# Optimization experiments

Measured on AMD Instinct MI355X. Metric: run time of the kernel, lower is better.

Reference implementation:

```python
import jax, jax.numpy as jnp
import numpy as np

E = 8      # number of experts (sublayers)
N = 8192   # tokens / batch rows
D = 1024   # sublayer input size (max_sublayer_input_size)
H = 2048   # sublayer output size
O = 1024   # output_encoding_size


def setup_inputs() -> dict:
    key = jax.random.key(0)
    k0, k1, k2, k3 = jax.random.split(key, 4)
    x_feat = jax.random.normal(k0, (N, D), dtype=jnp.float32)
    expert_idx = jax.random.randint(k1, (N,), 0, E)  # exclusive (top-1) routing
    # Stacked expert params: sublayers = Linear(D,H), encoders = Linear(H,O)
    W1 = jax.random.normal(k2, (E, D, H), dtype=jnp.float32) * (1.0 / np.sqrt(D))
    b1 = jnp.zeros((E, H), dtype=jnp.float32)
    W2 = jax.random.normal(k3, (E, H, O), dtype=jnp.float32) * (1.0 / np.sqrt(H))
    b2 = jnp.zeros((E, O), dtype=jnp.float32)
    return {"x_feat": x_feat, "W1": W1, "b1": b1, "W2": W2, "b2": b2,
            "expert_idx": expert_idx}


def reference(x_feat, W1, b1, W2, b2, expert_idx):
    # one-hot sublayer_mask (last E columns of the original x)
    onehot = jax.nn.one_hot(expert_idx, E, dtype=x_feat.dtype)  # [N, E]
    # Exclusive dispatch: each token goes through exactly one expert.
    # Structural loop over the fixed E experts; combine via the one-hot mask
    # (equivalent to the original gather -> sublayer -> encoder -> scatter).
    enc = jnp.zeros((x_feat.shape[0], O), dtype=x_feat.dtype)
    for i in range(E):
        h = x_feat @ W1[i] + b1[i]          # [N, H] sublayer
        y = h @ W2[i] + b2[i]               # [N, O] encoder
        enc = enc + onehot[:, i:i + 1] * y  # keep only rows routed to expert i
    # output = [encoded (O cols) | sublayer_mask (E cols)]
    return jnp.concatenate([enc, onehot], axis=1)
```

## Files before the change

### kernel.cpp

```cpp
#include <hip/hip_runtime.h>

#define NTOK 8192
#define DDIM 1024
#define HDIM 2048
#define ODIM 1024
#define NEXP 8
#define OUTW (ODIM + NEXP)
#define MT_MAX 64

typedef __bf16 bf16_t;
typedef bf16_t bf16x8 __attribute__((ext_vector_type(8)));
typedef bf16_t bf16x4 __attribute__((ext_vector_type(4)));
typedef float f32x4 __attribute__((ext_vector_type(4)));

__device__ __forceinline__ void gld_lds16(bf16_t* lds, const bf16_t* g) {
  __builtin_amdgcn_global_load_lds(
      (__attribute__((address_space(1))) void*)g,
      (__attribute__((address_space(3))) void*)lds, 16, 0, 0);
}

__global__ void route_kernel(const int* __restrict__ idx, float* __restrict__ out,
                             int* __restrict__ rank, int* cnt) {
  __shared__ int lcnt[NEXP];
  __shared__ int lbase[NEXP];
  int t = threadIdx.x;
  if (t < NEXP) lcnt[t] = 0;
  __syncthreads();
  int n = blockIdx.x * 256 + t;
  int e = idx[n];
  int lr = atomicAdd(&lcnt[e], 1);
  __syncthreads();
  if (t < NEXP) lbase[t] = atomicAdd(&cnt[t], lcnt[t]);
  __syncthreads();
  rank[n] = lbase[e] + lr;
  float* o = out + (size_t)n * OUTW + ODIM;
#pragma unroll
  for (int j = 0; j < NEXP; j++) o[j] = (j == e) ? 1.0f : 0.0f;
}

__device__ __forceinline__ void prefix_of(const int* cnt, int e, int& base, int& count) {
  base = 0; count = 0;
#pragma unroll
  for (int j = 0; j < NEXP; j++) {
    int c = cnt[j];
    if (j < e) base += c;
    if (j == e) count = c;
  }
}

__global__ void gather_kernel(const float* __restrict__ x, const int* __restrict__ idx,
                              const int* __restrict__ rank, const int* __restrict__ cnt,
                              bf16_t* __restrict__ xg, int* __restrict__ tok_of_pos) {
  int n = blockIdx.x;
  int e = idx[n];
  int base, count;
  prefix_of(cnt, e, base, count);
  int pos = base + rank[n];
  if (threadIdx.x == 0) tok_of_pos[pos] = n;
  float4 v = ((const float4*)(x + (size_t)n * DDIM))[threadIdx.x];
  bf16x4 o;
  o[0] = (bf16_t)v.x; o[1] = (bf16_t)v.y; o[2] = (bf16_t)v.z; o[3] = (bf16_t)v.w;
  *(bf16x4*)(xg + (size_t)pos * DDIM + threadIdx.x * 4) = o;
}

__global__ __launch_bounds__(256) void wtrans2_kernel(
    const float* __restrict__ s1, bf16_t* __restrict__ d1,
    const float* __restrict__ s2, bf16_t* __restrict__ d2) {
  __shared__ float t[128][65];
  int b = blockIdx.x;
  const float* src; bf16_t* dst; int R, C, bx, by, e;
  if (b < 2048) {
    src = s1; dst = d1; R = DDIM; C = HDIM;
    bx = b & 31; by = (b >> 5) & 7; e = b >> 8;
  } else {
    int b2 = b - 2048;
    src = s2; dst = d2; R = HDIM; C = ODIM;
    bx = b2 & 15; by = (b2 >> 4) & 15; e = b2 >> 8;
  }
  int c0 = bx * 64, r0g = by * 128;
  int tid = threadIdx.x;
  const float* s = src + (size_t)e * R * C;
#pragma unroll
  for (int p = 0; p < 8; p++) {
    int r = (tid >> 4) + p * 16;
    int c4 = (tid & 15) * 4;
    float4 v = *(const float4*)&s[(size_t)(r0g + r) * C + c0 + c4];
    t[r][c4 + 0] = v.x;
    t[r][c4 + 1] = v.y;
    t[r][c4 + 2] = v.z;
    t[r][c4 + 3] = v.w;
  }
  __syncthreads();
  bf16_t* d = dst + (size_t)e * R * C;
  int w = tid >> 6, l = tid & 63;
#pragma unroll
  for (int itc = 0; itc < 2; itc++) {
#pragma unroll
    for (int it2 = 0; it2 < 2; it2++) {
      int c = (l >> 3) + 8 * w + 32 * itc;
      int r0 = (l & 7) * 8 + 64 * it2;
      bf16x8 o;
#pragma unroll
      for (int j = 0; j < 8; j++) o[j] = (bf16_t)t[r0 + j][c];
      *(bf16x8*)&d[(size_t)(c0 + c) * R + r0g + r0] = o;
    }
  }
}

template <int KDIM, int NCOLS, int MTG, bool TO_BF16>
__global__ __launch_bounds__(256) void gemm_kernel(
    const bf16_t* __restrict__ A, const bf16_t* __restrict__ Bt,
    const float* __restrict__ bias,
    const int* __restrict__ cnt,
    const int* __restrict__ tok_of_pos,
    bf16_t* __restrict__ outb, float* __restrict__ outf) {
  constexpr int NT = NCOLS / 128;
  const int b = blockIdx.x;
  const int e = b & 7;
  int t = b >> 3;
  const int mtl = t % MTG;
  t /= MTG;
  const int nt = t % NT;
  const int g = t / NT;
  const int mt = g * MTG + mtl;

  int base, count;
  prefix_of(cnt, e, base, count);
  if (mt * 128 >= count) return;

  __shared__ bf16_t lA[128 * 32];
  __shared__ bf16_t lB[128 * 32];

  const int tid = threadIdx.x;
  const int lane = tid & 63;
  const int wave = tid >> 6;
  const int mrow = lane & 15;
  const int q = lane >> 4;
  const int wm = (wave & 1) * 64;
  const int wn = (wave >> 1) * 64;

  const bf16_t* pA[2];
  const bf16_t* pB[2];
#pragma unroll
  for (int s = 0; s < 2; s++) {
    int lrow = wave * 32 + s * 16 + (lane >> 2);
    int kq = (lane & 3) ^ (lrow & 3);
    int gr = base + mt * 128 + lrow;
    if (gr > NTOK - 1) gr = NTOK - 1;
    pA[s] = A + (size_t)gr * KDIM + kq * 8;
    int nrow = nt * 128 + lrow;
    pB[s] = Bt + ((size_t)e * NCOLS + nrow) * KDIM + kq * 8;
  }

  f32x4 acc[4][4] = {};
  const bf16_t* la0 = &lA[(wm + mrow) * 32 + ((q ^ (mrow & 3)) * 8)];
  const bf16_t* lb0 = &lB[(wn + mrow) * 32 + ((q ^ (mrow & 3)) * 8)];

  for (int kk = 0; kk < KDIM; kk += 32) {
#pragma unroll
    for (int s = 0; s < 2; s++) {
      gld_lds16(&lA[(wave * 2 + s) * 512], pA[s] + kk);
      gld_lds16(&lB[(wave * 2 + s) * 512], pB[s] + kk);
    }
    __syncthreads();
    bf16x8 af[4], bfr[4];
#pragma unroll
    for (int i = 0; i < 4; i++) {
      af[i]  = *(const bf16x8*)(la0 + i * 16 * 32);
      bfr[i] = *(const bf16x8*)(lb0 + i * 16 * 32);
    }
#pragma unroll
    for (int i = 0; i < 4; i++)
#pragma unroll
      for (int j = 0; j < 4; j++)
        acc[i][j] = __builtin_amdgcn_mfma_f32_16x16x32_bf16(af[i], bfr[j], acc[i][j], 0, 0, 0);
    __syncthreads();
  }

  const int mlimit = count - mt * 128;
  float bs[4];
#pragma unroll
  for (int j = 0; j < 4; j++)
    bs[j] = bias[(size_t)e * NCOLS + nt * 128 + wn + j * 16 + mrow];

#pragma unroll
  for (int i = 0; i < 4; i++) {
#pragma unroll
    for (int r = 0; r < 4; r++) {
      int ml = wm + i * 16 + q * 4 + r;
      if (ml < mlimit) {
        int prow = base + mt * 128 + ml;
        if constexpr (TO_BF16) {
          bf16_t* orow = outb + (size_t)prow * NCOLS;
#pragma unroll
          for (int j = 0; j < 4; j++)
            orow[nt * 128 + wn + j * 16 + mrow] = (bf16_t)(acc[i][j][r] + bs[j]);
        } else {
          int tok = tok_of_pos[prow];
          float* orow = outf + (size_t)tok * OUTW;
#pragma unroll
          for (int j = 0; j < 4; j++)
            orow[nt * 128 + wn + j * 16 + mrow] = acc[i][j][r] + bs[j];
        }
      }
    }
  }
}

extern "C" void kernel_launch(void* const* d_in, const int* in_sizes, int n_in,
                              void* d_out, int out_size, void* d_ws, size_t ws_size,
                              hipStream_t stream) {
  const float* x  = (const float*)d_in[0];
  const float* W1 = (const float*)d_in[1];
  const float* b1 = (const float*)d_in[2];
  const float* W2 = (const float*)d_in[3];
  const float* b2 = (const float*)d_in[4];
  const int* idx  = (const int*)d_in[5];
  float* out = (float*)d_out;

  char* ws = (char*)d_ws;
  bf16_t* xg  = (bf16_t*)(ws);
  bf16_t* hg  = (bf16_t*)(ws + 16777216);
  bf16_t* Wt1 = (bf16_t*)(ws + 50331648);
  bf16_t* Wt2 = (bf16_t*)(ws + 83886080);
  int* tok    = (int*)(ws + 117440512);
  int* rank   = (int*)(ws + 117473280);
  int* cnt    = (int*)(ws + 117506048);

  hipMemsetAsync(cnt, 0, NEXP * sizeof(int), stream);
  route_kernel<<<NTOK / 256, 256, 0, stream>>>(idx, out, rank, cnt);
  gather_kernel<<<NTOK, 256, 0, stream>>>(x, idx, rank, cnt, xg, tok);
  wtrans2_kernel<<<4096, 256, 0, stream>>>(W1, Wt1, W2, Wt2);
  gemm_kernel<DDIM, HDIM, 8, true>
      <<<NEXP * MT_MAX * (HDIM / 128), 256, 0, stream>>>(
      xg, Wt1, b1, cnt, tok, hg, nullptr);
  gemm_kernel<HDIM, ODIM, 4, false>
      <<<NEXP * MT_MAX * (ODIM / 128), 256, 0, stream>>>(
      hg, Wt2, b2, cnt, tok, nullptr, out);
}
```

Baseline: 311.2 us.

## Deepen GEMM K-step to 64 with XOR swizzle and merge prep kernels

The grouped expert GEMMs now stage a 64-wide K slice per iteration instead of 32. Each wave issues four 16-byte LDS loads with an 8-way XOR swizzle, and the compute runs two MFMA halves per sync. This halves the number of barrier pairs and loop iterations per tile, at the cost of doubling LDS use per block to 32 KB. Separately, the activation gather/convert and the weight transpose kernels are fused into one launch to save a kernel boundary and let the two jobs overlap.

After: 329.2 us. +5.8%, slower.

```diff
diff --git a/kernel.cpp b/kernel.cpp
--- a/kernel.cpp
+++ b/kernel.cpp
@@ -48,26 +48,31 @@
   }
 }
 
-__global__ void gather_kernel(const float* __restrict__ x, const int* __restrict__ idx,
-                              const int* __restrict__ rank, const int* __restrict__ cnt,
-                              bf16_t* __restrict__ xg, int* __restrict__ tok_of_pos) {
-  int n = blockIdx.x;
-  int e = idx[n];
-  int base, count;
-  prefix_of(cnt, e, base, count);
-  int pos = base + rank[n];
-  if (threadIdx.x == 0) tok_of_pos[pos] = n;
-  float4 v = ((const float4*)(x + (size_t)n * DDIM))[threadIdx.x];
-  bf16x4 o;
-  o[0] = (bf16_t)v.x; o[1] = (bf16_t)v.y; o[2] = (bf16_t)v.z; o[3] = (bf16_t)v.w;
-  *(bf16x4*)(xg + (size_t)pos * DDIM + threadIdx.x * 4) = o;
-}
-
-__global__ __launch_bounds__(256) void wtrans2_kernel(
+__global__ __launch_bounds__(256) void prep_kernel(
+    const float* __restrict__ x, const int* __restrict__ idx,
+    const int* __restrict__ rank, const int* __restrict__ cnt,
+    bf16_t* __restrict__ xg, int* __restrict__ tok_of_pos,
     const float* __restrict__ s1, bf16_t* __restrict__ d1,
     const float* __restrict__ s2, bf16_t* __restrict__ d2) {
   __shared__ float t[128][65];
   int b = blockIdx.x;
+  int tid = threadIdx.x;
+
+  if (b < NTOK) {
+    int n = b;
+    int e = idx[n];
+    int base, count;
+    prefix_of(cnt, e, base, count);
+    int pos = base + rank[n];
+    if (tid == 0) tok_of_pos[pos] = n;
+    float4 v = ((const float4*)(x + (size_t)n * DDIM))[tid];
+    bf16x4 o;
+    o[0] = (bf16_t)v.x; o[1] = (bf16_t)v.y; o[2] = (bf16_t)v.z; o[3] = (bf16_t)v.w;
+    *(bf16x4*)(xg + (size_t)pos * DDIM + tid * 4) = o;
+    return;
+  }
+
+  b -= NTOK;
   const float* src; bf16_t* dst; int R, C, bx, by, e;
   if (b < 2048) {
     src = s1; dst = d1; R = DDIM; C = HDIM;
@@ -78,7 +83,6 @@
     bx = b2 & 15; by = (b2 >> 4) & 15; e = b2 >> 8;
   }
   int c0 = bx * 64, r0g = by * 128;
-  int tid = threadIdx.x;
   const float* s = src + (size_t)e * R * C;
 #pragma unroll
   for (int p = 0; p < 8; p++) {
@@ -128,8 +132,8 @@
   prefix_of(cnt, e, base, count);
   if (mt * 128 >= count) return;
 
-  __shared__ bf16_t lA[128 * 32];
-  __shared__ bf16_t lB[128 * 32];
+  __shared__ bf16_t lA[128 * 64];
+  __shared__ bf16_t lB[128 * 64];
 
   const int tid = threadIdx.x;
   const int lane = tid & 63;
@@ -139,35 +143,49 @@
   const int wm = (wave & 1) * 64;
   const int wn = (wave >> 1) * 64;
 
-  const bf16_t* pA[2];
-  const bf16_t* pB[2];
-#pragma unroll
-  for (int s = 0; s < 2; s++) {
-    int lrow = wave * 32 + s * 16 + (lane >> 2);
-    int kq = (lane & 3) ^ (lrow & 3);
+  const bf16_t* pA[4];
+  const bf16_t* pB[4];
+#pragma unroll
+  for (int s = 0; s < 4; s++) {
+    int c = wave * 4 + s;
+    int lrow = c * 8 + (lane >> 3);
+    int qg = (lane & 7) ^ (lane >> 3);
     int gr = base + mt * 128 + lrow;
     if (gr > NTOK - 1) gr = NTOK - 1;
-    pA[s] = A + (size_t)gr * KDIM + kq * 8;
+    pA[s] = A + (size_t)gr * KDIM + qg * 8;
     int nrow = nt * 128 + lrow;
-    pB[s] = Bt + ((size_t)e * NCOLS + nrow) * KDIM + kq * 8;
+    pB[s] = Bt + ((size_t)e * NCOLS + nrow) * KDIM + qg * 8;
   }
 
   f32x4 acc[4][4] = {};
-  const bf16_t* la0 = &lA[(wm + mrow) * 32 + ((q ^ (mrow & 3)) * 8)];
-  const bf16_t* lb0 = &lB[(wn + mrow) * 32 + ((q ^ (mrow & 3)) * 8)];
-
-  for (int kk = 0; kk < KDIM; kk += 32) {
-#pragma unroll
-    for (int s = 0; s < 2; s++) {
-      gld_lds16(&lA[(wave * 2 + s) * 512], pA[s] + kk);
-      gld_lds16(&lB[(wave * 2 + s) * 512], pB[s] + kk);
+  const int m7 = mrow & 7;
+  const bf16_t* la0 = &lA[(wm + mrow) * 64 + ((q ^ m7) * 8)];
+  const bf16_t* la1 = &lA[(wm + mrow) * 64 + (((4 + q) ^ m7) * 8)];
+  const bf16_t* lb0 = &lB[(wn + mrow) * 64 + ((q ^ m7) * 8)];
+  const bf16_t* lb1 = &lB[(wn + mrow) * 64 + (((4 + q) ^ m7) * 8)];
+
+  for (int kk = 0; kk < KDIM; kk += 64) {
+#pragma unroll
+    for (int s = 0; s < 4; s++) {
+      gld_lds16(&lA[(wave * 4 + s) * 512], pA[s] + kk);
+      gld_lds16(&lB[(wave * 4 + s) * 512], pB[s] + kk);
     }
     __syncthreads();
     bf16x8 af[4], bfr[4];
 #pragma unroll
     for (int i = 0; i < 4; i++) {
-      af[i]  = *(const bf16x8*)(la0 + i * 16 * 32);
-      bfr[i] = *(const bf16x8*)(lb0 + i * 16 * 32);
+      af[i]  = *(const bf16x8*)(la0 + i * 16 * 64);
+      bfr[i] = *(const bf16x8*)(lb0 + i * 16 * 64);
+    }
+#pragma unroll
+    for (int i = 0; i < 4; i++)
+#pragma unroll
+      for (int j = 0; j < 4; j++)
+        acc[i][j] = __builtin_amdgcn_mfma_f32_16x16x32_bf16(af[i], bfr[j], acc[i][j], 0, 0, 0);
+#pragma unroll
+    for (int i = 0; i < 4; i++) {
+      af[i]  = *(const bf16x8*)(la1 + i * 16 * 64);
+      bfr[i] = *(const bf16x8*)(lb1 + i * 16 * 64);
     }
 #pragma unroll
     for (int i = 0; i < 4; i++)
@@ -229,8 +247,8 @@
 
   hipMemsetAsync(cnt, 0, NEXP * sizeof(int), stream);
   route_kernel<<<NTOK / 256, 256, 0, stream>>>(idx, out, rank, cnt);
-  gather_kernel<<<NTOK, 256, 0, stream>>>(x, idx, rank, cnt, xg, tok);
-  wtrans2_kernel<<<4096, 256, 0, stream>>>(W1, Wt1, W2, Wt2);
+  prep_kernel<<<NTOK + 4096, 256, 0, stream>>>(x, idx, rank, cnt, xg, tok,
+                                               W1, Wt1, W2, Wt2);
   gemm_kernel<DDIM, HDIM, 8, true>
       <<<NEXP * MT_MAX * (HDIM / 128), 256, 0, stream>>>(
       xg, Wt1, b1, cnt, tok, hg, nullptr);
```
